# Kernel optimization log

Measured on AMD Instinct MI355X. Metric: run time of the kernel, lower is better.

The kernel has to match this reference:

```python
import jax, jax.numpy as jnp
import numpy as np


def setup_inputs() -> dict:
    key = jax.random.key(0)
    k1, k2, k3 = jax.random.split(key, 3)
    B, L, H = 8, 2048, 256
    g = jax.random.normal(k1, (B, L, H), dtype=jnp.float32)
    # nn.Linear weights: stored as [out_features, in_features]
    WP = jax.random.normal(k2, (H, H), dtype=jnp.float32) * (1.0 / np.sqrt(H))
    W_out = jax.random.normal(k3, (H, 3 * H), dtype=jnp.float32) * (1.0 / np.sqrt(3 * H))
    b_out = jnp.zeros((H,), dtype=jnp.float32)
    return {"g": g, "WP": WP, "W_out": W_out, "b_out": b_out}


def reference(g, WP, W_out, b_out):
    # Wh = WP(g): [B, L, H] @ WP^T
    Wh = jnp.einsum("blh,oh->blo", g, WP)
    # s_t = bmm(Wh, g^T): [B, L, L]  (rows indexed by Wh positions, cols by g positions)
    s_t = jnp.einsum("bih,bjh->bij", Wh, g)
    # softmax over dim=1 (the first L axis, non-standard)
    a_t = jax.nn.softmax(s_t, axis=1)
    # c_t = bmm(a_t, g): [B, L, H]
    c_t = jnp.einsum("bij,bjh->bih", a_t, g)
    out = jnp.concatenate((g, c_t, g * c_t), axis=2)  # [B, L, 3H]
    out = jnp.einsum("blk,ok->blo", out, W_out) + b_out
    return jax.nn.relu(out)
```

## Files before the change

kernel.cpp:

```cpp
#include <hip/hip_runtime.h>
#include <math.h>

static constexpr int  Bb = 8;
static constexpr int  L  = 2048;
static constexpr int  H  = 256;
static constexpr long BL = (long)Bb * L;
static constexpr long LH = (long)L * H;
static constexpr long LL = (long)L * L;
static constexpr int  NCH = 16;

typedef __attribute__((ext_vector_type(8))) unsigned short u16x8;
typedef __attribute__((ext_vector_type(4))) unsigned short u16x4;
typedef __attribute__((ext_vector_type(8))) _Float16       f16x8;
typedef __attribute__((ext_vector_type(4))) float          f32x4;

__device__ __forceinline__ unsigned short f2hu(float x) {
    union { _Float16 h; unsigned short u; } v; v.h = (_Float16)x; return v.u;
}
__device__ __forceinline__ float hu2f(unsigned short u) {
    union { unsigned short u; _Float16 h; } v; v.u = u; return (float)v.h;
}
__device__ __forceinline__ void gl_lds16(const unsigned short* g, unsigned short* l) {
    __builtin_amdgcn_global_load_lds(
        (const __attribute__((address_space(1))) unsigned int*)g,
        (__attribute__((address_space(3))) unsigned int*)l, 16, 0, 0);
}

__global__ __launch_bounds__(256)
void cvt_g(const float* __restrict__ x, unsigned short* __restrict__ h)
{
    const long i = ((long)blockIdx.x * 256 + threadIdx.x) * 4;
    float4 v = *(const float4*)(x + i);
    u16x4 o;
    o[0] = f2hu(v.x); o[1] = f2hu(v.y); o[2] = f2hu(v.z); o[3] = f2hu(v.w);
    *(u16x4*)(h + i) = o;
}

__global__ __launch_bounds__(256)
void cvt_two(const float* __restrict__ x1, unsigned short* __restrict__ h1,
             const float* __restrict__ x2, unsigned short* __restrict__ h2)
{
    const float* x; unsigned short* hp; long base;
    if (blockIdx.x < 64) { x = x1; hp = h1; base = (long)blockIdx.x * 1024; }
    else { x = x2; hp = h2; base = (long)(blockIdx.x - 64) * 1024; }
    const long i = base + (long)threadIdx.x * 4;
    float4 v = *(const float4*)(x + i);
    u16x4 o;
    o[0] = f2hu(v.x); o[1] = f2hu(v.y); o[2] = f2hu(v.z); o[3] = f2hu(v.w);
    *(u16x4*)(hp + i) = o;
}

__global__ __launch_bounds__(256)
void transpose_h16(const unsigned short* __restrict__ in, unsigned short* __restrict__ out)
{
    __shared__ unsigned short T[32][33];
    const int b = blockIdx.z, j0 = blockIdx.x * 32, h0 = blockIdx.y * 32;
    const int t = threadIdx.x, r = t >> 3, c4 = (t & 7) << 2;
    const unsigned short* inb = in + (long)b * LH;
    unsigned short* outb = out + (long)b * LH;
    u16x4 v = *(const u16x4*)(inb + (long)(j0 + r) * H + h0 + c4);
#pragma unroll
    for (int e = 0; e < 4; ++e) T[r][c4 + e] = v[e];
    __syncthreads();
    u16x4 w;
#pragma unroll
    for (int e = 0; e < 4; ++e) w[e] = T[c4 + e][r];
    *(u16x4*)(outb + (long)(h0 + r) * L + j0 + c4) = w;
}

__global__ __launch_bounds__(256)
void col_stats_r(const float* __restrict__ pm, const float* __restrict__ pz,
                 float* __restrict__ rfac)
{
    const long idx = (long)blockIdx.x * 256 + threadIdx.x;
    const long b = idx / L, j = idx - b * L;
    const float* pmb = pm + b * (long)NCH * L + j;
    const float* pzb = pz + b * (long)NCH * L + j;
    float m = -1e30f;
#pragma unroll
    for (int c = 0; c < NCH; ++c) m = fmaxf(m, pmb[(long)c * L]);
    float z = 0.f;
#pragma unroll
    for (int c = 0; c < NCH; ++c) z += pzb[(long)c * L] * __expf(pmb[(long)c * L] - m);
    const float zi = 1.f / z;
    float* rb = rfac + b * (long)NCH * L + j;
#pragma unroll
    for (int c = 0; c < NCH; ++c) rb[(long)c * L] = __expf(pmb[(long)c * L] - m) * zi;
}

template<int MODE, int NSEG>
__global__ __launch_bounds__(256)
void mfma_nt(const unsigned short* A0, const unsigned short* A1, const unsigned short* A2,
             const unsigned short* B0, const unsigned short* B1, const unsigned short* B2,
             float* __restrict__ C, unsigned short* __restrict__ Ch,
             float* __restrict__ pm, float* __restrict__ pz,
             const float* __restrict__ bias,
             int N, int lda, int ldb,
             long strideA, long strideB, long strideC)
{
    __shared__ __align__(16) unsigned short As[128][32];
    __shared__ __align__(16) unsigned short Bs[128][32];
    __shared__ float smx[2][128];
    __shared__ float szx[2][128];
    __shared__ float colm[128];
    __shared__ __align__(16) unsigned short Ps[(MODE == 0) ? 128 : 1][136];
    const int tid  = threadIdx.x;
    const int wid  = tid >> 6, lane = tid & 63;
    const int wm   = wid >> 1, wn = wid & 1;
    const long b   = blockIdx.z;
    const int m0   = blockIdx.x * 128, n0 = blockIdx.y * 128;
    const int lrow = tid >> 2, lkc = (tid & 3) << 3;
    const int frow = lane & 15, fk = (lane >> 4) << 3;
    f32x4 acc[4][4];
#pragma unroll
    for (int i = 0; i < 4; ++i)
#pragma unroll
        for (int j = 0; j < 4; ++j) acc[i][j] = (f32x4){0.f, 0.f, 0.f, 0.f};

    const long abase = b * strideA, bbase = b * strideB;
    unsigned short* AsW = &As[0][0] + ((tid >> 6) << 9);
    unsigned short* BsW = &Bs[0][0] + ((tid >> 6) << 9);

    for (int seg = 0; seg < NSEG; ++seg) {
        const unsigned short* Ap = (seg == 0) ? A0 : ((seg == 1) ? A1 : A2);
        const unsigned short* Bp = (seg == 0) ? B0 : ((seg == 1) ? B1 : B2);
        for (int k0 = 0; k0 < 256; k0 += 32) {
            if (MODE == 1) {
                __syncthreads();
#pragma unroll
                for (int r = 0; r < 2; ++r) {
                    const int row = lrow + (r << 6);
                    u16x8 av;
                    if (seg == 2) {
                        const long off = (long)(m0 + row) * lda + k0 + lkc;
                        u16x8 gv = *(const u16x8*)(A0 + off);
                        u16x8 cv = *(const u16x8*)(A1 + off);
#pragma unroll
                        for (int e = 0; e < 8; ++e)
                            av[e] = f2hu(hu2f(gv[e]) * hu2f(cv[e]));
                    } else {
                        av = *(const u16x8*)(Ap + (long)(m0 + row) * lda + k0 + lkc);
                    }
                    *(u16x8*)&As[row][lkc] = av;
                    u16x8 bv = *(const u16x8*)(Bp + (long)(n0 + row) * ldb + k0 + lkc);
                    *(u16x8*)&Bs[row][lkc] = bv;
                }
                __syncthreads();
            } else {
                const unsigned short* Abase = Ap + abase + (long)m0 * lda + k0;
                const unsigned short* Bbase = Bp + bbase + (long)n0 * ldb + k0;
                __syncthreads();
#pragma unroll
                for (int r = 0; r < 2; ++r) {
                    gl_lds16(Abase + (long)(lrow + (r << 6)) * lda + lkc, AsW + (r << 11));
                    gl_lds16(Bbase + (long)(lrow + (r << 6)) * ldb + lkc, BsW + (r << 11));
                }
                __syncthreads();
            }
            f16x8 af[4], bfv[4];
#pragma unroll
            for (int i = 0; i < 4; ++i) af[i]  = *(const f16x8*)&As[wm * 64 + i * 16 + frow][fk];
#pragma unroll
            for (int j = 0; j < 4; ++j) bfv[j] = *(const f16x8*)&Bs[wn * 64 + j * 16 + frow][fk];
#pragma unroll
            for (int i = 0; i < 4; ++i)
#pragma unroll
                for (int j = 0; j < 4; ++j)
                    acc[i][j] = __builtin_amdgcn_mfma_f32_16x16x32_f16(af[i], bfv[j], acc[i][j], 0, 0, 0);
        }
    }

    if (MODE == 0) {
#pragma unroll
        for (int j = 0; j < 4; ++j) {
            float m = -1e30f;
#pragma unroll
            for (int i = 0; i < 4; ++i)
#pragma unroll
                for (int e = 0; e < 4; ++e) m = fmaxf(m, acc[i][j][e]);
            m = fmaxf(m, __shfl_xor(m, 16));
            m = fmaxf(m, __shfl_xor(m, 32));
            if ((lane >> 4) == 0) smx[wm][wn * 64 + j * 16 + frow] = m;
        }
        __syncthreads();
        if (tid < 128) colm[tid] = fmaxf(smx[0][tid], smx[1][tid]);
        __syncthreads();
#pragma unroll
        for (int j = 0; j < 4; ++j) {
            const int colL = wn * 64 + j * 16 + frow;
            const float mm = colm[colL];
            float z = 0.f;
#pragma unroll
            for (int i = 0; i < 4; ++i) {
                const int rl = wm * 64 + i * 16 + ((lane >> 4) << 2);
#pragma unroll
                for (int e = 0; e < 4; ++e) {
                    float p = __expf(acc[i][j][e] - mm);
                    z += p;
                    Ps[rl + e][colL] = f2hu(p);
                }
            }
            z += __shfl_xor(z, 16);
            z += __shfl_xor(z, 32);
            if ((lane >> 4) == 0) szx[wm][colL] = z;
        }
        __syncthreads();
        unsigned short* Pb = Ch + b * strideC;
        const int q = lane >> 4, c16 = lane & 15;
#pragma unroll
        for (int e2 = 0; e2 < 8; ++e2) {
            const int rl = e2 * 16 + wid * 4 + q;
            u16x8 v = *(const u16x8*)&Ps[rl][c16 * 8];
            *(u16x8*)(Pb + (long)(m0 + rl) * N + n0 + c16 * 8) = v;
        }
        if (tid < 128) {
            const long o = ((long)b * NCH + blockIdx.x) * L + n0 + tid;
            pm[o] = colm[tid];
            pz[o] = szx[0][tid] + szx[1][tid];
        }
    } else {
#pragma unroll
        for (int i = 0; i < 4; ++i)
#pragma unroll
            for (int j = 0; j < 4; ++j) {
                const int rbase = m0 + wm * 64 + i * 16 + ((lane >> 4) << 2);
                const int col   = n0 + wn * 64 + j * 16 + frow;
                if (MODE == 2) {
#pragma unroll
                    for (int e = 0; e < 4; ++e)
                        Ch[(long)(rbase + e) * N + col] = f2hu(acc[i][j][e]);
                } else {
                    float* Cb = C + b * strideC;
                    const float bv = bias[col];
#pragma unroll
                    for (int e = 0; e < 4; ++e)
                        Cb[(long)(rbase + e) * N + col] = fmaxf(acc[i][j][e] + bv, 0.f);
                }
            }
    }
}

__global__ __launch_bounds__(256)
void attn_av(const unsigned short* __restrict__ P, const float* __restrict__ rfac,
             const unsigned short* __restrict__ gT, unsigned short* __restrict__ ch)
{
    extern __shared__ unsigned short BsD[];
    const int t = threadIdx.x, b = blockIdx.z;
    const int i0 = blockIdx.x * 32;
    const int chunk = i0 >> 7;
    const int w = t >> 6, l = t & 63;
    const int frow = l & 15, fk = (l >> 4) << 3;
    const unsigned short* Pb  = P + (long)b * LL;
    const float* rrow = rfac + ((long)b * NCH + chunk) * L;
    const unsigned short* gTb = gT + (long)b * LH;
    unsigned short* cb = ch + (long)b * LH;

    const unsigned short* bsrc[4];
#pragma unroll
    for (int r = 0; r < 4; ++r) {
        const int rp  = r * 32 + (t >> 3);
        const int q16 = (t & 7) << 3;
        const int ua  = q16 ^ ((rp & 7) << 3);
        const int hh  = rp * 2 + (ua >> 5);
        bsrc[r] = gTb + (long)hh * L + (ua & 31);
    }
    int boff[4];
#pragma unroll
    for (int j4 = 0; j4 < 4; ++j4) {
        const int hrow = w * 64 + j4 * 16 + frow;
        const int rp = hrow >> 1;
        const int u  = ((hrow & 1) << 5) + fk;
        boff[j4] = rp * 64 + (u ^ ((rp & 7) << 3));
    }
    const unsigned short* prow0 = Pb + (long)(i0 + frow) * L + fk;
    const unsigned short* prow1 = Pb + (long)(i0 + 16 + frow) * L + fk;

    f32x4 acc[2][4];
#pragma unroll
    for (int i = 0; i < 2; ++i)
#pragma unroll
        for (int j = 0; j < 4; ++j) acc[i][j] = (f32x4){0.f, 0.f, 0.f, 0.f};

    u16x8 pA0, pA1, pB0, pB1;
    float4 rAa, rAb, rBa, rBb;

#define STAGE_B(BUF, J)                                                     \
    {                                                                       \
        unsigned short* dst = BsD + (BUF) * 8192 + w * 512;                 \
        _Pragma("unroll")                                                   \
        for (int r = 0; r < 4; ++r)                                         \
            gl_lds16(bsrc[r] + (J), dst + r * 2048);                        \
    }

    STAGE_B(0, 0)
    STAGE_B(1, 32)
    __builtin_amdgcn_sched_barrier(0);
    pA0 = *(const u16x8*)(prow0);          pA1 = *(const u16x8*)(prow1);
    rAa = *(const float4*)(rrow + fk);     rAb = *(const float4*)(rrow + fk + 4);
    pB0 = *(const u16x8*)(prow0 + 32);     pB1 = *(const u16x8*)(prow1 + 32);
    rBa = *(const float4*)(rrow + 32 + fk); rBb = *(const float4*)(rrow + 32 + fk + 4);
    __builtin_amdgcn_sched_barrier(0);
    asm volatile("s_waitcnt vmcnt(8)" ::: "memory");
    __builtin_amdgcn_sched_barrier(0);
    __builtin_amdgcn_s_barrier();

#define STEP(PH, C, P0V, P1V, RAV, RBV)                                     \
    {                                                                       \
        const int jS = ((C) + 2) * 32;                                      \
        if (jS < L) STAGE_B(((PH) + 2) & 3, jS)                             \
        __builtin_amdgcn_sched_barrier(0);                                  \
        f16x8 rh;                                                           \
        rh[0] = (_Float16)RAV.x; rh[1] = (_Float16)RAV.y;                   \
        rh[2] = (_Float16)RAV.z; rh[3] = (_Float16)RAV.w;                   \
        rh[4] = (_Float16)RBV.x; rh[5] = (_Float16)RBV.y;                   \
        rh[6] = (_Float16)RBV.z; rh[7] = (_Float16)RBV.w;                   \
        f16x8 a0 = *(f16x8*)&P0V * rh;                                      \
        f16x8 a1 = *(f16x8*)&P1V * rh;                                      \
        _Pragma("unroll")                                                   \
        for (int j4 = 0; j4 < 4; ++j4) {                                    \
            f16x8 bf = *(const f16x8*)(BsD + (PH) * 8192 + boff[j4]);       \
            acc[0][j4] = __builtin_amdgcn_mfma_f32_16x16x32_f16(a0, bf, acc[0][j4], 0, 0, 0); \
            acc[1][j4] = __builtin_amdgcn_mfma_f32_16x16x32_f16(a1, bf, acc[1][j4], 0, 0, 0); \
        }                                                                   \
        if (jS < L) {                                                       \
            P0V = *(const u16x8*)(prow0 + jS);                              \
            P1V = *(const u16x8*)(prow1 + jS);                              \
            RAV = *(const float4*)(rrow + jS + fk);                         \
            RBV = *(const float4*)(rrow + jS + fk + 4);                     \
        }                                                                   \
        __builtin_amdgcn_sched_barrier(0);                                  \
        if ((C) >= 61) { asm volatile("s_waitcnt vmcnt(0)" ::: "memory"); } \
        else           { asm volatile("s_waitcnt vmcnt(8)" ::: "memory"); } \
        __builtin_amdgcn_sched_barrier(0);                                  \
        __builtin_amdgcn_s_barrier();                                       \
    }

    for (int cc = 0; cc < 16; ++cc) {
        const int c0 = cc * 4;
        STEP(0, c0 + 0, pA0, pA1, rAa, rAb)
        STEP(1, c0 + 1, pB0, pB1, rBa, rBb)
        STEP(2, c0 + 2, pA0, pA1, rAa, rAb)
        STEP(3, c0 + 3, pB0, pB1, rBa, rBb)
    }
#undef STEP
#undef STAGE_B

#pragma unroll
    for (int i = 0; i < 2; ++i)
#pragma unroll
        for (int j = 0; j < 4; ++j) {
            const int rbase = i0 + i * 16 + ((l >> 4) << 2);
            const int col   = w * 64 + j * 16 + frow;
#pragma unroll
            for (int e = 0; e < 4; ++e)
                cb[(long)(rbase + e) * H + col] = f2hu(acc[i][j][e]);
        }
}

extern "C" void kernel_launch(void* const* d_in, const int* in_sizes, int n_in,
                              void* d_out, int out_size, void* d_ws, size_t ws_size,
                              hipStream_t stream)
{
    const float* g     = (const float*)d_in[0];
    const float* WP    = (const float*)d_in[1];
    const float* W_out = (const float*)d_in[2];
    const float* b_out = (const float*)d_in[3];
    float* out = (float*)d_out;

    char* w = (char*)d_ws;
    unsigned short* P    = (unsigned short*)w;
    unsigned short* gh   = (unsigned short*)(w + 67108864);
    unsigned short* ch   = (unsigned short*)(w + 75497472);
    unsigned short* gT   = (unsigned short*)(w + 83886080);
    unsigned short* Whh  = (unsigned short*)(w + 92274688);
    unsigned short* WPh  = (unsigned short*)(w + 100663296);
    unsigned short* Woh  = (unsigned short*)(w + 100794368);
    float*          pm   = (float*)(w + 101187584);
    float*          pz   = (float*)(w + 102236160);
    float*          rfac = (float*)(w + 103284736);

    cvt_g<<<dim3((int)(BL * H / 1024)), 256, 0, stream>>>(g, gh);
    cvt_two<<<dim3(256), 256, 0, stream>>>(WP, WPh, W_out, Woh);

    mfma_nt<2, 1><<<dim3((int)(BL / 128), H / 128, 1), 256, 0, stream>>>(
        gh, nullptr, nullptr, WPh, nullptr, nullptr, nullptr, Whh,
        nullptr, nullptr, nullptr, H, H, H, 0, 0, 0);

    mfma_nt<0, 1><<<dim3(L / 128, L / 128, Bb), 256, 0, stream>>>(
        Whh, nullptr, nullptr, gh, nullptr, nullptr, nullptr, P,
        pm, pz, nullptr, L, H, H, LH, LH, LL);

    col_stats_r<<<dim3((int)(BL / 256)), 256, 0, stream>>>(pm, pz, rfac);

    transpose_h16<<<dim3(L / 32, H / 32, Bb), 256, 0, stream>>>(gh, gT);

    attn_av<<<dim3(L / 32, 1, Bb), 256, 65536, stream>>>(P, rfac, gT, ch);

    mfma_nt<1, 3><<<dim3((int)(BL / 128), H / 128, 1), 256, 0, stream>>>(
        gh, ch, nullptr, Woh, Woh + 256, Woh + 512, out, nullptr,
        nullptr, nullptr, b_out, H, H, 3 * H, 0, 0, 0);
}
```

Baseline: 218.7 us.

## Stage P tiles and fp16 rfac in LDS and double-buffer gT in attn_av

The attn_av kernel now copies P tiles into a 4-deep LDS ring with 4-byte global_load_lds, replacing per-thread register loads. Each block converts its rfac row to fp16 once into LDS instead of converting float4 values every step. The gT staging drops from four LDS buffers to two, cutting dynamic LDS from 64 KB to 44 KB, so more blocks can be resident per CU. In exchange, the P loads use narrow 4-byte LDS-direct transfers and the B prefetch distance shrinks to one stage, which may expose more memory latency.

```diff
diff --git a/kernel.cpp b/kernel.cpp
--- a/kernel.cpp
+++ b/kernel.cpp
@@ -24,6 +24,11 @@
     __builtin_amdgcn_global_load_lds(
         (const __attribute__((address_space(1))) unsigned int*)g,
         (__attribute__((address_space(3))) unsigned int*)l, 16, 0, 0);
+}
+__device__ __forceinline__ void gl_lds4(const unsigned short* g, unsigned short* l) {
+    __builtin_amdgcn_global_load_lds(
+        (const __attribute__((address_space(1))) unsigned int*)g,
+        (__attribute__((address_space(3))) unsigned int*)l, 4, 0, 0);
 }
 
 __global__ __launch_bounds__(256)
@@ -244,7 +249,10 @@
 void attn_av(const unsigned short* __restrict__ P, const float* __restrict__ rfac,
              const unsigned short* __restrict__ gT, unsigned short* __restrict__ ch)
 {
-    extern __shared__ unsigned short BsD[];
+    extern __shared__ unsigned short LDSD[];
+    unsigned short* Bsh = LDSD;
+    unsigned short* Ash = LDSD + 16384;
+    unsigned short* Rs  = LDSD + 20480;
     const int t = threadIdx.x, b = blockIdx.z;
     const int i0 = blockIdx.x * 32;
     const int chunk = i0 >> 7;
@@ -261,19 +269,26 @@
         const int rp  = r * 32 + (t >> 3);
         const int q16 = (t & 7) << 3;
         const int ua  = q16 ^ ((rp & 7) << 3);
-        const int hh  = rp * 2 + (ua >> 5);
-        bsrc[r] = gTb + (long)hh * L + (ua & 31);
+        bsrc[r] = gTb + (long)(rp * 2 + (ua >> 5)) * L + (ua & 31);
+    }
+    const unsigned short* asrc[2];
+#pragma unroll
+    for (int ld = 0; ld < 2; ++ld) {
+        const int idx = t * 2 + ld * 512;
+        const int rp  = idx >> 6;
+        const int up  = (idx & 63) ^ ((rp & 7) << 3);
+        asrc[ld] = Pb + (long)(i0 + rp * 2 + (up >> 5)) * L + (up & 31);
     }
     int boff[4];
 #pragma unroll
     for (int j4 = 0; j4 < 4; ++j4) {
         const int hrow = w * 64 + j4 * 16 + frow;
         const int rp = hrow >> 1;
-        const int u  = ((hrow & 1) << 5) + fk;
-        boff[j4] = rp * 64 + (u ^ ((rp & 7) << 3));
-    }
-    const unsigned short* prow0 = Pb + (long)(i0 + frow) * L + fk;
-    const unsigned short* prow1 = Pb + (long)(i0 + 16 + frow) * L + fk;
+        boff[j4] = rp * 64 + ((((hrow & 1) << 5) + fk) ^ ((rp & 7) << 3));
+    }
+    const int arp   = frow >> 1;
+    const int aoff0 = arp * 64 + ((((frow & 1) << 5) + fk) ^ ((arp & 7) << 3));
+    const int aoff1 = aoff0 + 512;
 
     f32x4 acc[2][4];
 #pragma unroll
@@ -281,69 +296,65 @@
 #pragma unroll
         for (int j = 0; j < 4; ++j) acc[i][j] = (f32x4){0.f, 0.f, 0.f, 0.f};
 
-    u16x8 pA0, pA1, pB0, pB1;
-    float4 rAa, rAb, rBa, rBb;
-
-#define STAGE_B(BUF, J)                                                     \
-    {                                                                       \
-        unsigned short* dst = BsD + (BUF) * 8192 + w * 512;                 \
-        _Pragma("unroll")                                                   \
-        for (int r = 0; r < 4; ++r)                                         \
-            gl_lds16(bsrc[r] + (J), dst + r * 2048);                        \
+#define STAGE_B(BUF, J)                                                      \
+    {                                                                        \
+        unsigned short* d = Bsh + (BUF) * 8192 + w * 512;                    \
+        _Pragma("unroll")                                                    \
+        for (int r = 0; r < 4; ++r) gl_lds16(bsrc[r] + (J), d + r * 2048);   \
+    }
+#define STAGE_A(BUF, J)                                                      \
+    {                                                                        \
+        unsigned short* d = Ash + (BUF) * 1024 + w * 128;                    \
+        _Pragma("unroll")                                                    \
+        for (int ld = 0; ld < 2; ++ld) gl_lds4(asrc[ld] + (J), d + ld * 512);\
     }
 
     STAGE_B(0, 0)
-    STAGE_B(1, 32)
+    STAGE_A(0, 0)
+    STAGE_A(1, 32)
+    {
+        float4 ra = *(const float4*)(rrow + t * 8);
+        float4 rb = *(const float4*)(rrow + t * 8 + 4);
+        u16x8 rv;
+        rv[0] = f2hu(ra.x); rv[1] = f2hu(ra.y); rv[2] = f2hu(ra.z); rv[3] = f2hu(ra.w);
+        rv[4] = f2hu(rb.x); rv[5] = f2hu(rb.y); rv[6] = f2hu(rb.z); rv[7] = f2hu(rb.w);
+        *(u16x8*)&Rs[t * 8] = rv;
+    }
+    asm volatile("s_waitcnt vmcnt(2) lgkmcnt(0)" ::: "memory");
+    __builtin_amdgcn_s_barrier();
     __builtin_amdgcn_sched_barrier(0);
-    pA0 = *(const u16x8*)(prow0);          pA1 = *(const u16x8*)(prow1);
-    rAa = *(const float4*)(rrow + fk);     rAb = *(const float4*)(rrow + fk + 4);
-    pB0 = *(const u16x8*)(prow0 + 32);     pB1 = *(const u16x8*)(prow1 + 32);
-    rBa = *(const float4*)(rrow + 32 + fk); rBb = *(const float4*)(rrow + 32 + fk + 4);
-    __builtin_amdgcn_sched_barrier(0);
-    asm volatile("s_waitcnt vmcnt(8)" ::: "memory");
-    __builtin_amdgcn_sched_barrier(0);
-    __builtin_amdgcn_s_barrier();
-
-#define STEP(PH, C, P0V, P1V, RAV, RBV)                                     \
-    {                                                                       \
-        const int jS = ((C) + 2) * 32;                                      \
-        if (jS < L) STAGE_B(((PH) + 2) & 3, jS)                             \
-        __builtin_amdgcn_sched_barrier(0);                                  \
-        f16x8 rh;                                                           \
-        rh[0] = (_Float16)RAV.x; rh[1] = (_Float16)RAV.y;                   \
-        rh[2] = (_Float16)RAV.z; rh[3] = (_Float16)RAV.w;                   \
-        rh[4] = (_Float16)RBV.x; rh[5] = (_Float16)RBV.y;                   \
-        rh[6] = (_Float16)RBV.z; rh[7] = (_Float16)RBV.w;                   \
-        f16x8 a0 = *(f16x8*)&P0V * rh;                                      \
-        f16x8 a1 = *(f16x8*)&P1V * rh;                                      \
-        _Pragma("unroll")                                                   \
-        for (int j4 = 0; j4 < 4; ++j4) {                                    \
-            f16x8 bf = *(const f16x8*)(BsD + (PH) * 8192 + boff[j4]);       \
+
+#define STEP(K, C)                                                           \
+    {                                                                        \
+        const int jB = ((C) + 1) * 32, jA = ((C) + 2) * 32;                  \
+        if (jB < L) STAGE_B(((K) + 1) & 1, jB)                               \
+        if (jA < L) STAGE_A(((K) + 2) & 3, jA)                               \
+        f16x8 rh  = *(const f16x8*)&Rs[(C) * 32 + fk];                       \
+        f16x8 pa0 = *(const f16x8*)&Ash[((K) & 3) * 1024 + aoff0];           \
+        f16x8 pa1 = *(const f16x8*)&Ash[((K) & 3) * 1024 + aoff1];           \
+        f16x8 a0 = pa0 * rh, a1 = pa1 * rh;                                  \
+        _Pragma("unroll")                                                    \
+        for (int j4 = 0; j4 < 4; ++j4) {                                     \
+            f16x8 bf = *(const f16x8*)&Bsh[((K) & 1) * 8192 + boff[j4]];     \
             acc[0][j4] = __builtin_amdgcn_mfma_f32_16x16x32_f16(a0, bf, acc[0][j4], 0, 0, 0); \
             acc[1][j4] = __builtin_amdgcn_mfma_f32_16x16x32_f16(a1, bf, acc[1][j4], 0, 0, 0); \
-        }                                                                   \
-        if (jS < L) {                                                       \
-            P0V = *(const u16x8*)(prow0 + jS);                              \
-            P1V = *(const u16x8*)(prow1 + jS);                              \
-            RAV = *(const float4*)(rrow + jS + fk);                         \
-            RBV = *(const float4*)(rrow + jS + fk + 4);                     \
-        }                                                                   \
-        __builtin_amdgcn_sched_barrier(0);                                  \
-        if ((C) >= 61) { asm volatile("s_waitcnt vmcnt(0)" ::: "memory"); } \
-        else           { asm volatile("s_waitcnt vmcnt(8)" ::: "memory"); } \
-        __builtin_amdgcn_sched_barrier(0);                                  \
-        __builtin_amdgcn_s_barrier();                                       \
+        }                                                                    \
+        if (jA < L) { asm volatile("s_waitcnt vmcnt(2)" ::: "memory"); }     \
+        else        { asm volatile("s_waitcnt vmcnt(0)" ::: "memory"); }     \
+        __builtin_amdgcn_s_barrier();                                        \
+        __builtin_amdgcn_sched_barrier(0);                                   \
     }
 
     for (int cc = 0; cc < 16; ++cc) {
         const int c0 = cc * 4;
-        STEP(0, c0 + 0, pA0, pA1, rAa, rAb)
-        STEP(1, c0 + 1, pB0, pB1, rBa, rBb)
-        STEP(2, c0 + 2, pA0, pA1, rAa, rAb)
-        STEP(3, c0 + 3, pB0, pB1, rBa, rBb)
+        STEP(0, c0 + 0)
+        STEP(1, c0 + 1)
+        STEP(2, c0 + 2)
+        STEP(3, c0 + 3)
     }
 #undef STEP
 #undef STAGE_B
+#undef STAGE_A
 
 #pragma unroll
     for (int i = 0; i < 2; ++i)
@@ -394,7 +405,7 @@
 
     transpose_h16<<<dim3(L / 32, H / 32, Bb), 256, 0, stream>>>(gh, gT);
 
-    attn_av<<<dim3(L / 32, 1, Bb), 256, 65536, stream>>>(P, rfac, gT, ch);
+    attn_av<<<dim3(L / 32, 1, Bb), 256, 45056, stream>>>(P, rfac, gT, ch);
 
     mfma_nt<1, 3><<<dim3((int)(BL / 128), H / 128, 1), 256, 0, stream>>>(
         gh, ch, nullptr, Woh, Woh + 256, Woh + 512, out, nullptr,
```

New measurement: 197.2 us. -9.8%, faster.
